# Kernel optimization log

Measured on AMD Instinct MI355X. Metric: run time of the kernel, lower is better.

## Reference

```python
import jax, jax.numpy as jnp
import numpy as np


def soft_thresholding(x, a):
    # sh(x, a) = max(0, |x| - a) * sign(x) == relu(x - a) - relu(-x - a)
    return jax.nn.relu(x - a) - jax.nn.relu(-x - a)


def setup_inputs() -> dict:
    key = jax.random.key(0)
    kA, kb = jax.random.split(key)
    bs, m, n = 32, 256, 512
    A = jax.random.normal(kA, (bs, m, n), dtype=jnp.float32)
    b = jax.random.normal(kb, (bs, m), dtype=jnp.float32)
    return {"A": A, "b": b, "bs": bs, "iters": 1000}


def reference(A, b, bs, iters, alpha=0.02, beta=0.02):
    # A: (bs, m, n), b: (bs, m). PDHG iteration:
    #   x = sh(x - alpha * A^T u, alpha)
    m, n = A.shape[1], A.shape[2]
    x0 = jnp.zeros((bs, n), dtype=jnp.float32)
    u0 = jnp.zeros((bs, m), dtype=jnp.float32)

    def step(carry, _):
        x, u = carry
        x_new = soft_thresholding(x - alpha * jnp.einsum('bmn,bm->bn', A, u), alpha)
        u_new = u + beta * (jnp.einsum('bmn,bn->bm', A, 2.0 * x_new - x) - b)
        return (x_new, u_new), None

    (x, u), _ = jax.lax.scan(step, (x0, u0), None, length=iters)
    return x
```

## Files before the change

kernel.cpp:

```cpp
#include <hip/hip_runtime.h>

#define BS    32
#define MDIM  256
#define NDIM  512
#define ITERS 1000
#define WPB   4
#define BLK   512
#define ALPHA 0.02f
#define BETA  0.02f

#define ATS      520
#define BT_OFF   (32 * ATS)
#define SMEM_FL  (BT_OFF + 32)

#define SLAB_FL  (2 * BS * NDIM)

__device__ __forceinline__ unsigned ld_coh_u32(const void* p) {
  return __hip_atomic_load(reinterpret_cast<const unsigned*>(p),
                           __ATOMIC_RELAXED, __HIP_MEMORY_SCOPE_AGENT);
}
__device__ __forceinline__ void st_coh_u32(void* p, unsigned v) {
  __hip_atomic_store(reinterpret_cast<unsigned*>(p), v,
                     __ATOMIC_RELAXED, __HIP_MEMORY_SCOPE_AGENT);
}
__device__ __forceinline__ unsigned tagf(float v, unsigned tag) {
  return (__float_as_uint(v) & ~0xFFu) | tag;
}

__global__ __launch_bounds__(BLK, 1) void pdhg_kernel(
    const float* __restrict__ A, const float* __restrict__ Bvec,
    float* __restrict__ out, float* __restrict__ slab)
{
  __shared__ float smem[SMEM_FL];
  const int tid   = threadIdx.x;
  const int bid   = blockIdx.x;
  const int batch = bid & (BS - 1);
  const int slice = bid >> 5;
  const int lane  = tid & 63;
  const int widx  = tid >> 6;
  const int rowbase = slice * 128 + widx * 16;
  const int row_own = lane & 15;
  const int i_own   = rowbase + row_own;

  float acc[16][8];
#pragma unroll
  for (int r = 0; r < 16; ++r)
#pragma unroll
    for (int c = 0; c < 8; ++c) acc[r][c] = 0.f;
  float cacc = 0.f;

  const float* Ag = A + (size_t)batch * MDIM * NDIM;

  for (int mt = 0; mt < MDIM / 32; ++mt) {
#pragma unroll 4
    for (int q = 0; q < 8; ++q) {
      int f  = q * 512 + tid;
      int mm = f >> 7;
      int j  = (f & 127) << 2;
      float4 v = *reinterpret_cast<const float4*>(
          Ag + (size_t)(mt * 32 + mm) * NDIM + j);
      *reinterpret_cast<float4*>(&smem[mm * ATS + j]) = v;
    }
    if (tid < 32) smem[BT_OFF + tid] = Bvec[batch * MDIM + mt * 32 + tid];
    __syncthreads();

#pragma unroll 2
    for (int m = 0; m < 32; ++m) {
      const float* row = &smem[m * ATS];
      float4 a0 = *reinterpret_cast<const float4*>(row + rowbase);
      float4 a1 = *reinterpret_cast<const float4*>(row + rowbase + 4);
      float4 a2 = *reinterpret_cast<const float4*>(row + rowbase + 8);
      float4 a3 = *reinterpret_cast<const float4*>(row + rowbase + 12);
      float ai[16] = {a0.x,a0.y,a0.z,a0.w, a1.x,a1.y,a1.z,a1.w,
                      a2.x,a2.y,a2.z,a2.w, a3.x,a3.y,a3.z,a3.w};
      float aj[8];
#pragma unroll
      for (int c = 0; c < 8; ++c) aj[c] = row[64 * c + lane];
      float bm  = smem[BT_OFF + m];
      float aio = row[i_own];
#pragma unroll
      for (int r = 0; r < 16; ++r)
#pragma unroll
        for (int c = 0; c < 8; ++c) acc[r][c] = fmaf(ai[r], aj[c], acc[r][c]);
      cacc = fmaf(aio, bm, cacc);
    }
    __syncthreads();
  }

  float x = 0.f, t = 0.f;
  float*       myslot = slab + batch * NDIM + i_own;
  const float* myrd   = slab + batch * NDIM + tid;

  for (int k = 0; k < ITERS; ++k) {
    float y  = x - ALPHA * t;
    float xn = fmaxf(y - ALPHA, 0.f) - fmaxf(-y - ALPHA, 0.f);
    if (k == ITERS - 1) { x = xn; break; }

    const int      par = (k & 1) * BS * NDIM;
    const unsigned tag = (unsigned)(k + 1) & 0xFFu;
    float wv = 2.f * xn - x;
    x = xn;
    if (lane < 16) st_coh_u32(myslot + par, tagf(wv, tag));

    unsigned q;
    do { q = ld_coh_u32(myrd + par); } while ((q ^ tag) & 0xFFu);

    smem[tid] = __uint_as_float(q);
    __syncthreads();

    float wr[8];
#pragma unroll
    for (int c = 0; c < 8; ++c) wr[c] = smem[64 * c + lane];

    float S[16];
#pragma unroll
    for (int r = 0; r < 16; ++r) {
      float p = acc[r][0] * wr[0];
#pragma unroll
      for (int c = 1; c < 8; ++c) p = fmaf(acc[r][c], wr[c], p);
      S[r] = p;
    }

    const bool b0 = (lane & 1), b1 = (lane & 2), b2 = (lane & 4), b3 = (lane & 8);
    float T[8];
#pragma unroll
    for (int i = 0; i < 8; ++i) {
      float keep = b0 ? S[2*i+1] : S[2*i];
      float send = b0 ? S[2*i]   : S[2*i+1];
      T[i] = keep + __shfl_xor(send, 1);
    }
    float U[4];
#pragma unroll
    for (int i = 0; i < 4; ++i) {
      float keep = b1 ? T[2*i+1] : T[2*i];
      float send = b1 ? T[2*i]   : T[2*i+1];
      U[i] = keep + __shfl_xor(send, 2);
    }
    float V[2];
#pragma unroll
    for (int i = 0; i < 2; ++i) {
      float keep = b2 ? U[2*i+1] : U[2*i];
      float send = b2 ? U[2*i]   : U[2*i+1];
      V[i] = keep + __shfl_xor(send, 4);
    }
    float Wv;
    {
      float keep = b3 ? V[1] : V[0];
      float send = b3 ? V[0] : V[1];
      Wv = keep + __shfl_xor(send, 8);
    }
    Wv += __shfl_xor(Wv, 16);
    Wv += __shfl_xor(Wv, 32);

    t += BETA * (Wv - cacc);
  }

  if (lane < 16) out[(size_t)batch * NDIM + i_own] = x;
}

extern "C" void kernel_launch(void* const* d_in, const int* in_sizes, int n_in,
                              void* d_out, int out_size, void* d_ws, size_t ws_size,
                              hipStream_t stream) {
  const float* A = (const float*)d_in[0];
  const float* b = (const float*)d_in[1];
  float* out  = (float*)d_out;
  float* slab = (float*)d_ws;

  hipMemsetAsync(d_ws, 0, SLAB_FL * sizeof(float), stream);

  void* args[] = {(void*)&A, (void*)&b, (void*)&out, (void*)&slab};
  hipLaunchCooperativeKernel((const void*)pdhg_kernel, dim3(BS * WPB), dim3(BLK),
                             args, 0, stream);
}
```

Before: 1.676 ms.

## Interleave two batches per workgroup to overlap cross-block exchange latency

Each workgroup now holds Gram-matrix slices for two batches, with eight workgroups sharing a batch pair and each owning 64 rows. The iteration loop alternates between the two batches, and each batch's next-iterate store is issued right after its update. The goal is to hide the global-memory handshake latency of one batch behind the other batch's compute. In exchange, each batch now depends on eight producing workgroups instead of four, which could lengthen the spin waits.

```diff
diff --git a/kernel.cpp b/kernel.cpp
--- a/kernel.cpp
+++ b/kernel.cpp
@@ -4,14 +4,15 @@
 #define MDIM  256
 #define NDIM  512
 #define ITERS 1000
-#define WPB   4
 #define BLK   512
 #define ALPHA 0.02f
 #define BETA  0.02f
 
+#define NWG   128
+
 #define ATS      520
 #define BT_OFF   (32 * ATS)
-#define SMEM_FL  (BT_OFF + 32)
+#define SMEM_FL  21504
 
 #define SLAB_FL  (2 * BS * NDIM)
 
@@ -27,29 +28,16 @@
   return (__float_as_uint(v) & ~0xFFu) | tag;
 }
 
-__global__ __launch_bounds__(BLK, 1) void pdhg_kernel(
-    const float* __restrict__ A, const float* __restrict__ Bvec,
-    float* __restrict__ out, float* __restrict__ slab)
+__device__ __forceinline__ void build_G(
+    const float* __restrict__ Ag, const float* __restrict__ bg,
+    float (&Gacc)[8][8], float& cown, float* smem,
+    int tid, int lane, int rowbase, int i_own)
 {
-  __shared__ float smem[SMEM_FL];
-  const int tid   = threadIdx.x;
-  const int bid   = blockIdx.x;
-  const int batch = bid & (BS - 1);
-  const int slice = bid >> 5;
-  const int lane  = tid & 63;
-  const int widx  = tid >> 6;
-  const int rowbase = slice * 128 + widx * 16;
-  const int row_own = lane & 15;
-  const int i_own   = rowbase + row_own;
-
-  float acc[16][8];
-#pragma unroll
-  for (int r = 0; r < 16; ++r)
-#pragma unroll
-    for (int c = 0; c < 8; ++c) acc[r][c] = 0.f;
-  float cacc = 0.f;
-
-  const float* Ag = A + (size_t)batch * MDIM * NDIM;
+#pragma unroll
+  for (int r = 0; r < 8; ++r)
+#pragma unroll
+    for (int c = 0; c < 8; ++c) Gacc[r][c] = 0.f;
+  cown = 0.f;
 
   for (int mt = 0; mt < MDIM / 32; ++mt) {
 #pragma unroll 4
@@ -61,7 +49,7 @@
           Ag + (size_t)(mt * 32 + mm) * NDIM + j);
       *reinterpret_cast<float4*>(&smem[mm * ATS + j]) = v;
     }
-    if (tid < 32) smem[BT_OFF + tid] = Bvec[batch * MDIM + mt * 32 + tid];
+    if (tid < 32) smem[BT_OFF + tid] = bg[mt * 32 + tid];
     __syncthreads();
 
 #pragma unroll 2
@@ -69,93 +57,137 @@
       const float* row = &smem[m * ATS];
       float4 a0 = *reinterpret_cast<const float4*>(row + rowbase);
       float4 a1 = *reinterpret_cast<const float4*>(row + rowbase + 4);
-      float4 a2 = *reinterpret_cast<const float4*>(row + rowbase + 8);
-      float4 a3 = *reinterpret_cast<const float4*>(row + rowbase + 12);
-      float ai[16] = {a0.x,a0.y,a0.z,a0.w, a1.x,a1.y,a1.z,a1.w,
-                      a2.x,a2.y,a2.z,a2.w, a3.x,a3.y,a3.z,a3.w};
+      float ai[8] = {a0.x,a0.y,a0.z,a0.w, a1.x,a1.y,a1.z,a1.w};
       float aj[8];
 #pragma unroll
       for (int c = 0; c < 8; ++c) aj[c] = row[64 * c + lane];
       float bm  = smem[BT_OFF + m];
       float aio = row[i_own];
 #pragma unroll
-      for (int r = 0; r < 16; ++r)
-#pragma unroll
-        for (int c = 0; c < 8; ++c) acc[r][c] = fmaf(ai[r], aj[c], acc[r][c]);
-      cacc = fmaf(aio, bm, cacc);
+      for (int r = 0; r < 8; ++r)
+#pragma unroll
+        for (int c = 0; c < 8; ++c) Gacc[r][c] = fmaf(ai[r], aj[c], Gacc[r][c]);
+      cown = fmaf(aio, bm, cown);
     }
     __syncthreads();
   }
-
-  float x = 0.f, t = 0.f;
-  float*       myslot = slab + batch * NDIM + i_own;
-  const float* myrd   = slab + batch * NDIM + tid;
-
-  for (int k = 0; k < ITERS; ++k) {
-    float y  = x - ALPHA * t;
+}
+
+__device__ __forceinline__ void phase(
+    const float (&Gacc)[8][8], float cown, float& x, float& t,
+    const float* myrd, float* myslot, float* wbuf,
+    int tid, int lane, int par, unsigned tag, int npar, unsigned ntag,
+    bool do_store)
+{
+  unsigned q;
+  do { q = ld_coh_u32(myrd + par); } while ((q ^ tag) & 0xFFu);
+  wbuf[tid] = __uint_as_float(q);
+  __syncthreads();
+
+  float wr[8];
+#pragma unroll
+  for (int c = 0; c < 8; ++c) wr[c] = wbuf[64 * c + lane];
+
+  float S[8];
+#pragma unroll
+  for (int r = 0; r < 8; ++r) {
+    float p = Gacc[r][0] * wr[0];
+#pragma unroll
+    for (int c = 1; c < 8; ++c) p = fmaf(Gacc[r][c], wr[c], p);
+    S[r] = p;
+  }
+
+  const bool b0 = lane & 1, b1 = lane & 2, b2 = lane & 4;
+  float T[4];
+#pragma unroll
+  for (int i = 0; i < 4; ++i) {
+    float keep = b0 ? S[2*i+1] : S[2*i];
+    float send = b0 ? S[2*i]   : S[2*i+1];
+    T[i] = keep + __shfl_xor(send, 1);
+  }
+  float U[2];
+#pragma unroll
+  for (int i = 0; i < 2; ++i) {
+    float keep = b1 ? T[2*i+1] : T[2*i];
+    float send = b1 ? T[2*i]   : T[2*i+1];
+    U[i] = keep + __shfl_xor(send, 2);
+  }
+  float Wv;
+  {
+    float keep = b2 ? U[1] : U[0];
+    float send = b2 ? U[0] : U[1];
+    Wv = keep + __shfl_xor(send, 4);
+  }
+  Wv += __shfl_xor(Wv, 8);
+  Wv += __shfl_xor(Wv, 16);
+  Wv += __shfl_xor(Wv, 32);
+
+  t += BETA * (Wv - cown);
+  float y  = x - ALPHA * t;
+  float xn = fmaxf(y - ALPHA, 0.f) - fmaxf(-y - ALPHA, 0.f);
+  float wv = 2.f * xn - x;
+  x = xn;
+  if (do_store && lane < 8) st_coh_u32(myslot + npar, tagf(wv, ntag));
+}
+
+__global__ __launch_bounds__(BLK, 1) void pdhg_kernel(
+    const float* __restrict__ A, const float* __restrict__ Bvec,
+    float* __restrict__ out, float* __restrict__ slab)
+{
+  __shared__ float smem[SMEM_FL];
+  const int tid    = threadIdx.x;
+  const int bid    = blockIdx.x;
+  const int g      = bid >> 3;
+  const int s      = bid & 7;
+  const int batchA = 2 * g;
+  const int batchB = 2 * g + 1;
+  const int lane   = tid & 63;
+  const int widx   = tid >> 6;
+  const int rowbase = s * 64 + widx * 8;
+  const int i_own   = rowbase + (lane & 7);
+
+  float accA[8][8], accB[8][8];
+  float cA, cB;
+  build_G(A + (size_t)batchA * MDIM * NDIM, Bvec + batchA * MDIM,
+          accA, cA, smem, tid, lane, rowbase, i_own);
+  build_G(A + (size_t)batchB * MDIM * NDIM, Bvec + batchB * MDIM,
+          accB, cB, smem, tid, lane, rowbase, i_own);
+
+  float xA = 0.f, tA = 0.f, xB = 0.f, tB = 0.f;
+  const float* myrdA = slab + batchA * NDIM + tid;
+  const float* myrdB = slab + batchB * NDIM + tid;
+  float* myslotA = slab + batchA * NDIM + i_own;
+  float* myslotB = slab + batchB * NDIM + i_own;
+
+  {
+    float y = xA - ALPHA * tA;
     float xn = fmaxf(y - ALPHA, 0.f) - fmaxf(-y - ALPHA, 0.f);
-    if (k == ITERS - 1) { x = xn; break; }
-
-    const int      par = (k & 1) * BS * NDIM;
-    const unsigned tag = (unsigned)(k + 1) & 0xFFu;
-    float wv = 2.f * xn - x;
-    x = xn;
-    if (lane < 16) st_coh_u32(myslot + par, tagf(wv, tag));
-
-    unsigned q;
-    do { q = ld_coh_u32(myrd + par); } while ((q ^ tag) & 0xFFu);
-
-    smem[tid] = __uint_as_float(q);
-    __syncthreads();
-
-    float wr[8];
-#pragma unroll
-    for (int c = 0; c < 8; ++c) wr[c] = smem[64 * c + lane];
-
-    float S[16];
-#pragma unroll
-    for (int r = 0; r < 16; ++r) {
-      float p = acc[r][0] * wr[0];
-#pragma unroll
-      for (int c = 1; c < 8; ++c) p = fmaf(acc[r][c], wr[c], p);
-      S[r] = p;
-    }
-
-    const bool b0 = (lane & 1), b1 = (lane & 2), b2 = (lane & 4), b3 = (lane & 8);
-    float T[8];
-#pragma unroll
-    for (int i = 0; i < 8; ++i) {
-      float keep = b0 ? S[2*i+1] : S[2*i];
-      float send = b0 ? S[2*i]   : S[2*i+1];
-      T[i] = keep + __shfl_xor(send, 1);
-    }
-    float U[4];
-#pragma unroll
-    for (int i = 0; i < 4; ++i) {
-      float keep = b1 ? T[2*i+1] : T[2*i];
-      float send = b1 ? T[2*i]   : T[2*i+1];
-      U[i] = keep + __shfl_xor(send, 2);
-    }
-    float V[2];
-#pragma unroll
-    for (int i = 0; i < 2; ++i) {
-      float keep = b2 ? U[2*i+1] : U[2*i];
-      float send = b2 ? U[2*i]   : U[2*i+1];
-      V[i] = keep + __shfl_xor(send, 4);
-    }
-    float Wv;
-    {
-      float keep = b3 ? V[1] : V[0];
-      float send = b3 ? V[0] : V[1];
-      Wv = keep + __shfl_xor(send, 8);
-    }
-    Wv += __shfl_xor(Wv, 16);
-    Wv += __shfl_xor(Wv, 32);
-
-    t += BETA * (Wv - cacc);
-  }
-
-  if (lane < 16) out[(size_t)batch * NDIM + i_own] = x;
+    float wv = 2.f * xn - xA; xA = xn;
+    if (lane < 8) st_coh_u32(myslotA, tagf(wv, 1u));
+  }
+  {
+    float y = xB - ALPHA * tB;
+    float xn = fmaxf(y - ALPHA, 0.f) - fmaxf(-y - ALPHA, 0.f);
+    float wv = 2.f * xn - xB; xB = xn;
+    if (lane < 8) st_coh_u32(myslotB, tagf(wv, 1u));
+  }
+
+  for (int j = 0; j < ITERS - 1; ++j) {
+    const int      par  = (j & 1) * BS * NDIM;
+    const unsigned tag  = (unsigned)(j + 1) & 0xFFu;
+    const int      npar = ((j + 1) & 1) * BS * NDIM;
+    const unsigned ntag = (unsigned)(j + 2) & 0xFFu;
+    const bool     ds   = (j < ITERS - 2);
+    phase(accA, cA, xA, tA, myrdA, myslotA, smem,       tid, lane,
+          par, tag, npar, ntag, ds);
+    phase(accB, cB, xB, tB, myrdB, myslotB, smem + 512, tid, lane,
+          par, tag, npar, ntag, ds);
+  }
+
+  if (lane < 8) {
+    out[(size_t)batchA * NDIM + i_own] = xA;
+    out[(size_t)batchB * NDIM + i_own] = xB;
+  }
 }
 
 extern "C" void kernel_launch(void* const* d_in, const int* in_sizes, int n_in,
@@ -169,6 +201,6 @@
   hipMemsetAsync(d_ws, 0, SLAB_FL * sizeof(float), stream);
 
   void* args[] = {(void*)&A, (void*)&b, (void*)&out, (void*)&slab};
-  hipLaunchCooperativeKernel((const void*)pdhg_kernel, dim3(BS * WPB), dim3(BLK),
+  hipLaunchCooperativeKernel((const void*)pdhg_kernel, dim3(NWG), dim3(BLK),
                              args, 0, stream);
 }
```

Measured after the change: 2.251 ms. 1.34x slower.

## Repartition Gram tile per wavefront and reduce partial sums across waves in LDS

Applied to the files above, without the earlier changes.

Each wavefront now holds all 128 block rows against its own 64-column slice of the Gram matrix, instead of 16 rows against all 512 columns. The polled w values are broadcast within the wave by shuffles rather than staged through LDS before a barrier. Partial row sums are combined across the 8 waves through a padded LDS buffer, and one lane in four finishes the update. This shortens the shuffle reduction chain and moves the single per-iteration barrier after the dot product, at the cost of an LDS cross-wave reduction and a serialized owner step.

```diff
diff --git a/kernel.cpp b/kernel.cpp
--- a/kernel.cpp
+++ b/kernel.cpp
@@ -4,14 +4,18 @@
 #define MDIM  256
 #define NDIM  512
 #define ITERS 1000
-#define WPB   4
 #define BLK   512
+#define NWG   128
 #define ALPHA 0.02f
 #define BETA  0.02f
 
+
 #define ATS      520
 #define BT_OFF   (32 * ATS)
-#define SMEM_FL  (BT_OFF + 32)
+#define C_OFF    (BT_OFF + 32)
+#define P_OFF    0
+#define PSTRIDE  12
+#define SMEM_FL  21504
 
 #define SLAB_FL  (2 * BS * NDIM)
 
@@ -38,9 +42,11 @@
   const int slice = bid >> 5;
   const int lane  = tid & 63;
   const int widx  = tid >> 6;
-  const int rowbase = slice * 128 + widx * 16;
-  const int row_own = lane & 15;
-  const int i_own   = rowbase + row_own;
+  const int rg    = lane >> 3;
+  const int cg    = lane & 7;
+
+  const int ibase = 128 * slice + 16 * rg;
+  const int jbase = 64 * widx + 8 * cg;
 
   float acc[16][8];
 #pragma unroll
@@ -67,61 +73,69 @@
 #pragma unroll 2
     for (int m = 0; m < 32; ++m) {
       const float* row = &smem[m * ATS];
-      float4 a0 = *reinterpret_cast<const float4*>(row + rowbase);
-      float4 a1 = *reinterpret_cast<const float4*>(row + rowbase + 4);
-      float4 a2 = *reinterpret_cast<const float4*>(row + rowbase + 8);
-      float4 a3 = *reinterpret_cast<const float4*>(row + rowbase + 12);
+      float4 a0 = *reinterpret_cast<const float4*>(row + ibase);
+      float4 a1 = *reinterpret_cast<const float4*>(row + ibase + 4);
+      float4 a2 = *reinterpret_cast<const float4*>(row + ibase + 8);
+      float4 a3 = *reinterpret_cast<const float4*>(row + ibase + 12);
       float ai[16] = {a0.x,a0.y,a0.z,a0.w, a1.x,a1.y,a1.z,a1.w,
                       a2.x,a2.y,a2.z,a2.w, a3.x,a3.y,a3.z,a3.w};
-      float aj[8];
-#pragma unroll
-      for (int c = 0; c < 8; ++c) aj[c] = row[64 * c + lane];
-      float bm  = smem[BT_OFF + m];
-      float aio = row[i_own];
+      float4 j0 = *reinterpret_cast<const float4*>(row + jbase);
+      float4 j1 = *reinterpret_cast<const float4*>(row + jbase + 4);
+      float aj[8] = {j0.x,j0.y,j0.z,j0.w, j1.x,j1.y,j1.z,j1.w};
+      float bm = smem[BT_OFF + m];
 #pragma unroll
       for (int r = 0; r < 16; ++r)
 #pragma unroll
         for (int c = 0; c < 8; ++c) acc[r][c] = fmaf(ai[r], aj[c], acc[r][c]);
-      cacc = fmaf(aio, bm, cacc);
+      if (tid < 128) cacc = fmaf(row[128 * slice + tid], bm, cacc);
     }
     __syncthreads();
   }
+  if (tid < 128) smem[C_OFF + tid] = cacc;
+  __syncthreads();
 
+  const bool owner = (tid & 3) == 0;
+  const int  Rloc  = tid >> 2;
+  const float c_reg = owner ? smem[C_OFF + Rloc] : 0.f;
   float x = 0.f, t = 0.f;
-  float*       myslot = slab + batch * NDIM + i_own;
+
+  float*       myslot = slab + batch * NDIM + 128 * slice + Rloc;
   const float* myrd   = slab + batch * NDIM + tid;
 
   for (int k = 0; k < ITERS; ++k) {
-    float y  = x - ALPHA * t;
-    float xn = fmaxf(y - ALPHA, 0.f) - fmaxf(-y - ALPHA, 0.f);
+    float xn = 0.f;
+    if (owner) {
+      float y = x - ALPHA * t;
+      xn = fmaxf(y - ALPHA, 0.f) - fmaxf(-y - ALPHA, 0.f);
+    }
     if (k == ITERS - 1) { x = xn; break; }
 
     const int      par = (k & 1) * BS * NDIM;
     const unsigned tag = (unsigned)(k + 1) & 0xFFu;
-    float wv = 2.f * xn - x;
-    x = xn;
-    if (lane < 16) st_coh_u32(myslot + par, tagf(wv, tag));
+    if (owner) {
+      float wv_ = 2.f * xn - x;
+      x = xn;
+      st_coh_u32(myslot + par, tagf(wv_, tag));
+    }
 
     unsigned q;
     do { q = ld_coh_u32(myrd + par); } while ((q ^ tag) & 0xFFu);
+    float w_own = __uint_as_float(q);
 
-    smem[tid] = __uint_as_float(q);
-    __syncthreads();
-
-    float wr[8];
+    float wv[8];
 #pragma unroll
-    for (int c = 0; c < 8; ++c) wr[c] = smem[64 * c + lane];
+    for (int c = 0; c < 8; ++c) wv[c] = __shfl(w_own, 8 * cg + c);
 
     float S[16];
 #pragma unroll
     for (int r = 0; r < 16; ++r) {
-      float p = acc[r][0] * wr[0];
+      float p = acc[r][0] * wv[0];
 #pragma unroll
-      for (int c = 1; c < 8; ++c) p = fmaf(acc[r][c], wr[c], p);
+      for (int c = 1; c < 8; ++c) p = fmaf(acc[r][c], wv[c], p);
       S[r] = p;
     }
 
-    const bool b0 = (lane & 1), b1 = (lane & 2), b2 = (lane & 4), b3 = (lane & 8);
+    const bool b0 = (lane & 1), b1 = (lane & 2), b2 = (lane & 4);
     float T[8];
 #pragma unroll
     for (int i = 0; i < 8; ++i) {
@@ -143,19 +157,22 @@
       float send = b2 ? U[2*i]   : U[2*i+1];
       V[i] = keep + __shfl_xor(send, 4);
     }
-    float Wv;
-    {
-      float keep = b3 ? V[1] : V[0];
-      float send = b3 ? V[0] : V[1];
-      Wv = keep + __shfl_xor(send, 8);
+
+    smem[P_OFF + (16 * rg + cg)     * PSTRIDE + widx] = V[0];
+    smem[P_OFF + (16 * rg + 8 + cg) * PSTRIDE + widx] = V[1];
+    __syncthreads();
+
+    if (owner) {
+      const float* pp = &smem[P_OFF + Rloc * PSTRIDE];
+      float4 pa = *reinterpret_cast<const float4*>(pp);
+      float4 pb = *reinterpret_cast<const float4*>(pp + 4);
+      float s8 = (pa.x + pa.y) + (pa.z + pa.w) +
+                 (pb.x + pb.y) + (pb.z + pb.w);
+      t += BETA * (s8 - c_reg);
     }
-    Wv += __shfl_xor(Wv, 16);
-    Wv += __shfl_xor(Wv, 32);
-
-    t += BETA * (Wv - cacc);
   }
 
-  if (lane < 16) out[(size_t)batch * NDIM + i_own] = x;
+  if (owner) out[(size_t)batch * NDIM + 128 * slice + Rloc] = x;
 }
 
 extern "C" void kernel_launch(void* const* d_in, const int* in_sizes, int n_in,
@@ -169,6 +186,6 @@
   hipMemsetAsync(d_ws, 0, SLAB_FL * sizeof(float), stream);
 
   void* args[] = {(void*)&A, (void*)&b, (void*)&out, (void*)&slab};
-  hipLaunchCooperativeKernel((const void*)pdhg_kernel, dim3(BS * WPB), dim3(BLK),
+  hipLaunchCooperativeKernel((const void*)pdhg_kernel, dim3(NWG), dim3(BLK),
                              args, 0, stream);
 }
```

Measured after the change: 1.525 ms. -9.0%, faster.
